# Performance work log

Hardware: AMD Instinct MI355X
Metric: run time of the kernel (lower is better)

The kernel has to match this reference:

```python
import jax, jax.numpy as jnp
import numpy as np

D = 768
NH = 8
HD = D // NH
DFF = 2048
EPS = 1e-5


def _layer_norm(x, g, b):
    mu = jnp.mean(x, axis=-1, keepdims=True)
    var = jnp.mean(jnp.square(x - mu), axis=-1, keepdims=True)
    return (x - mu) * jax.lax.rsqrt(var + EPS) * g + b


def setup_inputs() -> dict:
    key = jax.random.key(0)
    ks = jax.random.split(key, 16)
    B, L = 2, 2048
    s = 0.02
    return {
        "x": jax.random.normal(ks[0], (B, L, D), jnp.float32),
        "attn_bias": jax.random.normal(ks[1], (B, L, L), jnp.float32),
        "in_proj_w": jax.random.normal(ks[2], (3 * D, D), jnp.float32) * s,
        "in_proj_b": jnp.zeros((3 * D,), jnp.float32),
        "out_w": jax.random.normal(ks[3], (D, D), jnp.float32) * s,
        "out_b": jnp.zeros((D,), jnp.float32),
        "W1": jax.random.normal(ks[4], (DFF, D), jnp.float32) * s,
        "b1": jnp.zeros((DFF,), jnp.float32),
        "W2": jax.random.normal(ks[5], (D, DFF), jnp.float32) * s,
        "b2": jnp.zeros((D,), jnp.float32),
        "g1": jnp.ones((D,), jnp.float32),
        "be1": jnp.zeros((D,), jnp.float32),
        "g2": jnp.ones((D,), jnp.float32),
        "be2": jnp.zeros((D,), jnp.float32),
    }


def reference(x, attn_bias, in_proj_w, in_proj_b, out_w, out_b,
              W1, b1, W2, b2, g1, be1, g2, be2):
    B, L, _ = x.shape
    # fused qkv projection (torch nn.MultiheadAttention in_proj)
    qkv = x @ in_proj_w.T + in_proj_b          # [B, L, 3D]
    q, k, v = jnp.split(qkv, 3, axis=-1)
    q = q.reshape(B, L, NH, HD).transpose(0, 2, 1, 3)  # [B, nH, L, hd]
    k = k.reshape(B, L, NH, HD).transpose(0, 2, 1, 3)
    v = v.reshape(B, L, NH, HD).transpose(0, 2, 1, 3)
    scale = 1.0 / jnp.sqrt(jnp.asarray(HD, x.dtype))
    scores = jnp.einsum("bhqd,bhkd->bhqk", q * scale, k)
    scores = scores + attn_bias[:, None, :, :]         # broadcast over heads == expand
    attn = jax.nn.softmax(scores, axis=-1)
    ctx = jnp.einsum("bhqk,bhkd->bhqd", attn, v)       # [B, nH, L, hd]
    ctx = ctx.transpose(0, 2, 1, 3).reshape(B, L, D)
    attn_out = ctx @ out_w.T + out_b
    x = _layer_norm(x + attn_out, g1, be1)
    h = jax.nn.gelu(x @ W1.T + b1, approximate=False)  # torch default GELU = erf
    ff = h @ W2.T + b2
    return _layer_norm(x + ff, g2, be2)
```

## Files before the change

kernel.cpp:

```cpp
#include <hip/hip_runtime.h>
#include <hip/hip_bf16.h>
#include <math.h>

typedef __bf16 bf16;
typedef __attribute__((ext_vector_type(8))) __bf16 bf16x8;
typedef __attribute__((ext_vector_type(4))) __bf16 bf16x4;
typedef __attribute__((ext_vector_type(2))) __bf16 bf16x2;
typedef __attribute__((ext_vector_type(4))) float f32x4;

#define LOG2E 1.4426950408889634f

__device__ __forceinline__ void gload16(const bf16* g, bf16* l) {
  __builtin_amdgcn_global_load_lds(
      (const __attribute__((address_space(1))) void*)g,
      (__attribute__((address_space(3))) void*)l, 16, 0, 0);
}

__device__ __forceinline__ unsigned packbf2(float a, float b) {
  bf16x2 v = { (bf16)a, (bf16)b };
  return __builtin_bit_cast(unsigned, v);
}

struct CastSegs { const float* src[5]; bf16* dst[5]; };

__global__ void fused_cast_kernel(CastSegs segs) {
  const int e0 = 786432, e1 = 1228800, e2 = 1376256, e3 = 1769472, e4 = 2162688;
  int i = blockIdx.x * blockDim.x + threadIdx.x;
  int stride = gridDim.x * blockDim.x;
  for (; i < e4; i += stride) {
    int s = 0, base = 0;
    if (i >= e0) { s = 1; base = e0; }
    if (i >= e1) { s = 2; base = e1; }
    if (i >= e2) { s = 3; base = e2; }
    if (i >= e3) { s = 4; base = e3; }
    float4 v = ((const float4*)segs.src[s])[i - base];
    bf16x4 o = { (bf16)v.x, (bf16)v.y, (bf16)v.z, (bf16)v.w };
    ((bf16x4*)segs.dst[s])[i - base] = o;
  }
}

template<int MODE>
__launch_bounds__(256)
__global__ void gemm_kernel(const bf16* __restrict__ A, const bf16* __restrict__ W,
                            const float* __restrict__ bias, bf16* __restrict__ vt,
                            void* __restrict__ out, int K, int O) {
  __shared__ bf16 As[128 * 64];
  __shared__ bf16 Bs[128 * 64];
  const int t    = threadIdx.x;
  const int lane = t & 63;
  const int wave = t >> 6;
  const int wr = (wave >> 1) * 64;
  const int wc = (wave & 1) * 64;
  const int n0 = blockIdx.y * 128;
  const int o0 = blockIdx.x * 128;

  f32x4 zero = {0.f, 0.f, 0.f, 0.f};
  f32x4 acc[4][4];
#pragma unroll
  for (int m = 0; m < 4; m++)
#pragma unroll
    for (int n = 0; n < 4; n++) acc[m][n] = zero;

  const int fr  = lane & 15;
  const int fg8 = (lane >> 4) * 8;

  for (int k0 = 0; k0 < K; k0 += 64) {
    __syncthreads();
#pragma unroll
    for (int c = 0; c < 4; c++) {
      int f = c * 256 + t;
      int row = f >> 3;
      int col = (f & 7) * 8;
      gload16(&A[(size_t)(n0 + row) * K + k0 + col], &As[f * 8]);
      gload16(&W[(size_t)(o0 + row) * K + k0 + col], &Bs[f * 8]);
    }
    __syncthreads();
#pragma unroll
    for (int kf = 0; kf < 2; kf++) {
      bf16x8 a[4], b[4];
#pragma unroll
      for (int m = 0; m < 4; m++) a[m] = *(const bf16x8*)&As[(wr + m * 16 + fr) * 64 + kf * 32 + fg8];
#pragma unroll
      for (int n = 0; n < 4; n++) b[n] = *(const bf16x8*)&Bs[(wc + n * 16 + fr) * 64 + kf * 32 + fg8];
#pragma unroll
      for (int m = 0; m < 4; m++)
#pragma unroll
        for (int n = 0; n < 4; n++)
          acc[m][n] = __builtin_amdgcn_mfma_f32_16x16x32_bf16(a[m], b[n], acc[m][n], 0, 0, 0);
    }
  }

  const int fg4 = (lane >> 4) * 4;
#pragma unroll
  for (int m = 0; m < 4; m++) {
#pragma unroll
    for (int n = 0; n < 4; n++) {
      int col = o0 + wc + n * 16 + fr;
      float bv = bias[col];
      if constexpr (MODE == 3) {
        if (col >= 1536) {
          int c = col - 1536;
          int h = c / 96;
          int hd = c - h * 96;
          int row0 = n0 + wr + m * 16 + fg4;
          int b = row0 >> 11;
          int token = row0 & 2047;
          bf16x4 ov;
#pragma unroll
          for (int r = 0; r < 4; r++) ov[r] = (bf16)(acc[m][n][r] + bv);
          *(bf16x4*)&vt[((size_t)((b * 8 + h) * 96 + hd)) * 2048 + token] = ov;
          continue;
        }
      }
#pragma unroll
      for (int r = 0; r < 4; r++) {
        int row = n0 + wr + m * 16 + fg4 + r;
        float v = acc[m][n][r] + bv;
        if constexpr (MODE == 2) {
          v = 0.5f * v * (1.0f + erff(v * 0.70710678118654752f));
          ((bf16*)out)[(size_t)row * O + col] = (bf16)v;
        } else {
          ((bf16*)out)[(size_t)row * O + col] = (bf16)v;
        }
      }
    }
  }
}

__launch_bounds__(256)
__global__ void gemmW_kernel(const bf16* __restrict__ A, const bf16* __restrict__ W,
                             const float* __restrict__ bias, const float* __restrict__ res,
                             float* __restrict__ out, int K, int O) {
  __shared__ bf16 As[128 * 64];
  __shared__ bf16 Bs[64 * 64];
  const int t    = threadIdx.x;
  const int lane = t & 63;
  const int wave = t >> 6;
  const int wr = wave * 32;
  const int n0 = blockIdx.y * 128;
  const int o0 = blockIdx.x * 64;

  f32x4 zero = {0.f, 0.f, 0.f, 0.f};
  f32x4 acc[2][4];
#pragma unroll
  for (int m = 0; m < 2; m++)
#pragma unroll
    for (int n = 0; n < 4; n++) acc[m][n] = zero;

  const int fr  = lane & 15;
  const int fg8 = (lane >> 4) * 8;

  for (int k0 = 0; k0 < K; k0 += 64) {
    __syncthreads();
#pragma unroll
    for (int c = 0; c < 4; c++) {
      int f = c * 256 + t;
      int row = f >> 3;
      int col = (f & 7) * 8;
      gload16(&A[(size_t)(n0 + row) * K + k0 + col], &As[f * 8]);
    }
#pragma unroll
    for (int c = 0; c < 2; c++) {
      int f = c * 256 + t;
      int row = f >> 3;
      int col = (f & 7) * 8;
      gload16(&W[(size_t)(o0 + row) * K + k0 + col], &Bs[f * 8]);
    }
    __syncthreads();
#pragma unroll
    for (int kf = 0; kf < 2; kf++) {
      bf16x8 a[2], b[4];
#pragma unroll
      for (int m = 0; m < 2; m++) a[m] = *(const bf16x8*)&As[(wr + m * 16 + fr) * 64 + kf * 32 + fg8];
#pragma unroll
      for (int n = 0; n < 4; n++) b[n] = *(const bf16x8*)&Bs[(n * 16 + fr) * 64 + kf * 32 + fg8];
#pragma unroll
      for (int m = 0; m < 2; m++)
#pragma unroll
        for (int n = 0; n < 4; n++)
          acc[m][n] = __builtin_amdgcn_mfma_f32_16x16x32_bf16(a[m], b[n], acc[m][n], 0, 0, 0);
    }
  }

  const int fg4 = (lane >> 4) * 4;
#pragma unroll
  for (int m = 0; m < 2; m++) {
#pragma unroll
    for (int n = 0; n < 4; n++) {
      int col = o0 + n * 16 + fr;
      float bv = bias[col];
#pragma unroll
      for (int r = 0; r < 4; r++) {
        int row = n0 + wr + m * 16 + fg4 + r;
        float v = acc[m][n][r] + bv + res[(size_t)row * O + col];
        out[(size_t)row * O + col] = v;
      }
    }
  }
}

__launch_bounds__(256, 2)
__global__ void attn_kernel(const bf16* __restrict__ qkv, const bf16* __restrict__ vt,
                            const float* __restrict__ bias, float* __restrict__ opart,
                            float* __restrict__ ml) {
  __shared__ bf16 Ks[64 * 104];
  __shared__ bf16 Vs[96 * 72];
  const int t    = threadIdx.x;
  const int lane = t & 63;
  const int wave = t >> 6;
  const int qb = blockIdx.x, h = blockIdx.y;
  const int half = blockIdx.z & 1, b = blockIdx.z >> 1;
  const int kvstart = half * 1024;
  const int q0 = qb * 128 + wave * 32;
  const int fq = lane & 15;
  const int g  = lane >> 4;
  const size_t base = (size_t)b * 2048 * 2304;

  bf16x8 qf[2][3];
#pragma unroll
  for (int ss = 0; ss < 2; ss++) {
    const bf16* qp = qkv + base + (size_t)(q0 + ss * 16 + fq) * 2304 + h * 96;
#pragma unroll
    for (int f = 0; f < 3; f++) qf[ss][f] = *(const bf16x8*)(qp + f * 32 + g * 8);
  }

  const int krow = t >> 2, kcb = (t & 3) * 24;
  const bf16* kbase = qkv + base + (size_t)kvstart * 2304 + 768 + h * 96;
  const bf16* vbase = vt + (size_t)((b * 8 + h) * 96) * 2048 + kvstart;

  bf16x8 kreg[3], vreg[3];
#pragma unroll
  for (int i = 0; i < 3; i++) {
    kreg[i] = *(const bf16x8*)(kbase + (size_t)krow * 2304 + kcb + i * 8);
    int c = t + 256 * i;
    vreg[i] = *(const bf16x8*)(vbase + (size_t)(c >> 3) * 2048 + (c & 7) * 8);
  }

  float m_run[2] = {-1e30f, -1e30f}, l_run[2] = {0.f, 0.f};
  f32x4 zero = {0.f, 0.f, 0.f, 0.f};
  f32x4 o_acc[2][6];
#pragma unroll
  for (int ss = 0; ss < 2; ss++)
#pragma unroll
    for (int i = 0; i < 6; i++) o_acc[ss][i] = zero;

  const float scale = 0.10206207261596575f;
  const float* bp[2];
  bp[0] = bias + ((size_t)b * 2048 + q0 + fq) * 2048 + kvstart;
  bp[1] = bp[0] + (size_t)16 * 2048;

  bf16x8 pb[2][2];

  for (int kv0 = 0; kv0 < 1024; kv0 += 64) {
    if (kv0) __syncthreads();
    *(bf16x8*)&Ks[krow * 104 + kcb]      = kreg[0];
    *(bf16x8*)&Ks[krow * 104 + kcb + 8]  = kreg[1];
    *(bf16x8*)&Ks[krow * 104 + kcb + 16] = kreg[2];
#pragma unroll
    for (int i = 0; i < 3; i++) {
      int c = t + 256 * i;
      *(bf16x8*)&Vs[(c >> 3) * 72 + (c & 7) * 8] = vreg[i];
    }
    if (kv0 + 64 < 1024) {
      int nx = kv0 + 64;
#pragma unroll
      for (int i = 0; i < 3; i++) {
        kreg[i] = *(const bf16x8*)(kbase + (size_t)(nx + krow) * 2304 + kcb + i * 8);
        int c = t + 256 * i;
        vreg[i] = *(const bf16x8*)(vbase + (size_t)(c >> 3) * 2048 + nx + (c & 7) * 8);
      }
    }
    __builtin_amdgcn_sched_barrier(0);
    __syncthreads();

    float4 bf[2][4];
#pragma unroll
    for (int ss = 0; ss < 2; ss++)
#pragma unroll
      for (int kvt = 0; kvt < 4; kvt++)
        bf[ss][kvt] = *(const float4*)(bp[ss] + kv0 + kvt * 16 + g * 4);

    f32x4 s[2][4];
#pragma unroll
    for (int kvt = 0; kvt < 4; kvt++) {
      s[0][kvt] = zero;
      s[1][kvt] = zero;
#pragma unroll
      for (int f = 0; f < 3; f++) {
        bf16x8 kfr = *(const bf16x8*)&Ks[(kvt * 16 + fq) * 104 + f * 32 + g * 8];
        s[0][kvt] = __builtin_amdgcn_mfma_f32_16x16x32_bf16(kfr, qf[0][f], s[0][kvt], 0, 0, 0);
        s[1][kvt] = __builtin_amdgcn_mfma_f32_16x16x32_bf16(kfr, qf[1][f], s[1][kvt], 0, 0, 0);
      }
    }

#pragma unroll
    for (int ss = 0; ss < 2; ss++) {
      float p[4][4];
      float vmax = -1e30f;
#pragma unroll
      for (int kvt = 0; kvt < 4; kvt++)
#pragma unroll
        for (int r = 0; r < 4; r++) {
          float sv = fmaf(s[ss][kvt][r], scale, (&bf[ss][kvt].x)[r]);
          p[kvt][r] = sv;
          vmax = fmaxf(vmax, sv);
        }
      vmax = fmaxf(vmax, __shfl_xor(vmax, 16));
      vmax = fmaxf(vmax, __shfl_xor(vmax, 32));
      if (!__all(vmax <= m_run[ss] + 8.0f)) {
        float m_new = fmaxf(m_run[ss], vmax);
        float corr = exp2f((m_run[ss] - m_new) * LOG2E);
        l_run[ss] *= corr;
#pragma unroll
        for (int i = 0; i < 6; i++)
#pragma unroll
          for (int r = 0; r < 4; r++) o_acc[ss][i][r] *= corr;
        m_run[ss] = m_new;
      }
      float rsum = 0.f;
      uint2 d[4];
#pragma unroll
      for (int kvt = 0; kvt < 4; kvt++) {
        float e0 = exp2f((p[kvt][0] - m_run[ss]) * LOG2E);
        float e1 = exp2f((p[kvt][1] - m_run[ss]) * LOG2E);
        float e2 = exp2f((p[kvt][2] - m_run[ss]) * LOG2E);
        float e3 = exp2f((p[kvt][3] - m_run[ss]) * LOG2E);
        rsum += (e0 + e1) + (e2 + e3);
        d[kvt].x = packbf2(e0, e1);
        d[kvt].y = packbf2(e2, e3);
      }
      rsum += __shfl_xor(rsum, 16);
      rsum += __shfl_xor(rsum, 32);
      l_run[ss] += rsum;

      bool glow = (g < 2);
      uint2 snd0 = glow ? d[1] : d[0];
      uint2 snd1 = glow ? d[3] : d[2];
      uint2 r0, r1;
      r0.x = __shfl_xor(snd0.x, 32); r0.y = __shfl_xor(snd0.y, 32);
      r1.x = __shfl_xor(snd1.x, 32); r1.y = __shfl_xor(snd1.y, 32);
      uint2 k0 = glow ? d[0] : d[1];
      uint2 k1 = glow ? d[2] : d[3];
      bool sendk = ((g ^ (g >> 1)) & 1);
      uint2 s0 = sendk ? k0 : r0;
      uint2 s1 = sendk ? k1 : r1;
      uint2 q0_, q1_;
      q0_.x = __shfl_xor(s0.x, 16); q0_.y = __shfl_xor(s0.y, 16);
      q1_.x = __shfl_xor(s1.x, 16); q1_.y = __shfl_xor(s1.y, 16);
      uint2 kept0 = sendk ? r0 : k0;
      uint2 kept1 = sendk ? r1 : k1;
      bool godd = (g & 1);
      uint2 lo0 = godd ? q0_ : kept0;
      uint2 hi0 = godd ? kept0 : q0_;
      uint2 lo1 = godd ? q1_ : kept1;
      uint2 hi1 = godd ? kept1 : q1_;
      uint4 u0 = { lo0.x, lo0.y, hi0.x, hi0.y };
      uint4 u1 = { lo1.x, lo1.y, hi1.x, hi1.y };
      pb[ss][0] = __builtin_bit_cast(bf16x8, u0);
      pb[ss][1] = __builtin_bit_cast(bf16x8, u1);
    }

#pragma unroll
    for (int kf = 0; kf < 2; kf++) {
#pragma unroll
      for (int ht = 0; ht < 6; ht++) {
        bf16x8 vfr = *(const bf16x8*)&Vs[(ht * 16 + fq) * 72 + kf * 32 + g * 8];
        o_acc[0][ht] = __builtin_amdgcn_mfma_f32_16x16x32_bf16(vfr, pb[0][kf], o_acc[0][ht], 0, 0, 0);
        o_acc[1][ht] = __builtin_amdgcn_mfma_f32_16x16x32_bf16(vfr, pb[1][kf], o_acc[1][ht], 0, 0, 0);
      }
    }
  }

#pragma unroll
  for (int ss = 0; ss < 2; ss++) {
    int q = q0 + ss * 16 + fq;
    float* op = opart + (size_t)half * (16 * 2048 * 96) + ((size_t)(b * 8 + h) * 2048 + q) * 96;
    float* mlp = ml + ((size_t)half * 32768 + (size_t)(b * 8 + h) * 2048 + q) * 2;
#pragma unroll
    for (int ht = 0; ht < 6; ht++)
      *(f32x4*)&op[ht * 16 + g * 4] = o_acc[ss][ht];
    if (g == 0) { mlp[0] = m_run[ss]; mlp[1] = l_run[ss]; }
  }
}

__launch_bounds__(256)
__global__ void attn_combine_kernel(const float* __restrict__ opart, const float* __restrict__ ml,
                                    bf16* __restrict__ ctx) {
  int idx = blockIdx.x * blockDim.x + threadIdx.x;
  if (idx >= 786432) return;
  int e = idx * 4;
  int bh = e / (2048 * 96);
  int rem = e - bh * (2048 * 96);
  int q = rem / 96;
  int hd = rem - q * 96;
  const float* op0 = opart;
  const float* op1 = opart + (size_t)16 * 2048 * 96;
  float4 o1 = *(const float4*)&op0[e];
  float4 o2 = *(const float4*)&op1[e];
  const float* ml0 = ml + (size_t)(bh * 2048 + q) * 2;
  const float* ml1 = ml0 + (size_t)32768 * 2;
  float m1 = ml0[0], l1 = ml0[1];
  float m2 = ml1[0], l2 = ml1[1];
  float M = fmaxf(m1, m2);
  float w1 = exp2f((m1 - M) * LOG2E);
  float w2 = exp2f((m2 - M) * LOG2E);
  float inv = 1.0f / (l1 * w1 + l2 * w2);
  int b = bh >> 3, h = bh & 7;
  bf16x4 o;
  o[0] = (bf16)((o1.x * w1 + o2.x * w2) * inv);
  o[1] = (bf16)((o1.y * w1 + o2.y * w2) * inv);
  o[2] = (bf16)((o1.z * w1 + o2.z * w2) * inv);
  o[3] = (bf16)((o1.w * w1 + o2.w * w2) * inv);
  *(bf16x4*)&ctx[((size_t)b * 2048 + q) * 768 + h * 96 + hd] = o;
}

__launch_bounds__(256)
__global__ void ln_kernel(const float* in, const float* __restrict__ gamma,
                          const float* __restrict__ beta, float* outf, bf16* outb) {
  const int row = blockIdx.x;
  const int t = threadIdx.x;
  const float* rp = in + (size_t)row * 768;
  float v[3];
#pragma unroll
  for (int i = 0; i < 3; i++) v[i] = rp[t + 256 * i];
  float s = v[0] + v[1] + v[2];
  float ss = v[0] * v[0] + v[1] * v[1] + v[2] * v[2];
#pragma unroll
  for (int off = 1; off < 64; off <<= 1) {
    s += __shfl_xor(s, off);
    ss += __shfl_xor(ss, off);
  }
  __shared__ float red[8];
  if ((t & 63) == 0) { red[(t >> 6) * 2] = s; red[(t >> 6) * 2 + 1] = ss; }
  __syncthreads();
  s = red[0] + red[2] + red[4] + red[6];
  ss = red[1] + red[3] + red[5] + red[7];
  float mu = s * (1.0f / 768.0f);
  float var = ss * (1.0f / 768.0f) - mu * mu;
  float rs = rsqrtf(var + 1e-5f);
#pragma unroll
  for (int i = 0; i < 3; i++) {
    int col = t + 256 * i;
    float y = (v[i] - mu) * rs * gamma[col] + beta[col];
    outf[(size_t)row * 768 + col] = y;
    if (outb) outb[(size_t)row * 768 + col] = (bf16)y;
  }
}

extern "C" void kernel_launch(void* const* d_in, const int* in_sizes, int n_in,
                              void* d_out, int out_size, void* d_ws, size_t ws_size,
                              hipStream_t stream) {
  (void)in_sizes; (void)n_in; (void)out_size; (void)ws_size;
  const float* x     = (const float*)d_in[0];
  const float* ab    = (const float*)d_in[1];
  const float* w_qkv = (const float*)d_in[2];
  const float* b_qkv = (const float*)d_in[3];
  const float* w_out = (const float*)d_in[4];
  const float* b_out = (const float*)d_in[5];
  const float* W1    = (const float*)d_in[6];
  const float* b1    = (const float*)d_in[7];
  const float* W2    = (const float*)d_in[8];
  const float* b2    = (const float*)d_in[9];
  const float* g1    = (const float*)d_in[10];
  const float* be1   = (const float*)d_in[11];
  const float* g2    = (const float*)d_in[12];
  const float* be2   = (const float*)d_in[13];
  float* outf = (float*)d_out;

  char* p = (char*)d_ws;
  bf16* xb    = (bf16*)p;  p += (size_t)4096 * 768 * 2;
  bf16* qkv   = (bf16*)p;  p += (size_t)4096 * 2304 * 2;
  bf16* ctx   = (bf16*)p;  p += (size_t)4096 * 768 * 2;
  float* x1f  = (float*)p; p += (size_t)4096 * 768 * 4;
  bf16* x1b   = (bf16*)p;  p += (size_t)4096 * 768 * 2;
  bf16* hbuf  = (bf16*)p;  p += (size_t)4096 * 2048 * 2;
  bf16* wqkvb = (bf16*)p;  p += (size_t)2304 * 768 * 2;
  bf16* woutb = (bf16*)p;  p += (size_t)768 * 768 * 2;
  bf16* w1b   = (bf16*)p;  p += (size_t)2048 * 768 * 2;
  bf16* w2b   = (bf16*)p;  p += (size_t)768 * 2048 * 2;
  float* opart = (float*)p; p += (size_t)2 * 16 * 2048 * 96 * 4;
  float* mlb   = (float*)p; p += (size_t)2 * 32768 * 2 * 4;
  bf16* vtb   = (bf16*)x1f;

  CastSegs segs;
  segs.src[0] = x;     segs.dst[0] = xb;
  segs.src[1] = w_qkv; segs.dst[1] = wqkvb;
  segs.src[2] = w_out; segs.dst[2] = woutb;
  segs.src[3] = W1;    segs.dst[3] = w1b;
  segs.src[4] = W2;    segs.dst[4] = w2b;
  fused_cast_kernel<<<2048, 256, 0, stream>>>(segs);

  gemm_kernel<3><<<dim3(18, 32), 256, 0, stream>>>(xb, wqkvb, b_qkv, vtb, qkv, 768, 2304);
  attn_kernel<<<dim3(16, 8, 4), 256, 0, stream>>>(qkv, vtb, ab, opart, mlb);
  attn_combine_kernel<<<3072, 256, 0, stream>>>(opart, mlb, ctx);
  gemmW_kernel<<<dim3(12, 32), 256, 0, stream>>>(ctx, woutb, b_out, x, outf, 768, 768);
  ln_kernel<<<4096, 256, 0, stream>>>(outf, g1, be1, x1f, x1b);
  gemm_kernel<2><<<dim3(16, 32), 256, 0, stream>>>(x1b, w1b, b1, nullptr, hbuf, 768, 2048);
  gemmW_kernel<<<dim3(12, 32), 256, 0, stream>>>(hbuf, w2b, b2, x1f, outf, 2048, 768);
  ln_kernel<<<4096, 256, 0, stream>>>(outf, g2, be2, outf, nullptr);
}
```

Measured before the change: 219.9 us.

## Double-buffer K/V tiles and software-pipeline QK^T with previous PV in attention

The attention kernel gets double-buffered shared memory for K and V tiles and a software-pipelined loop. Each iteration issues the QK^T MFMAs for the current tile together with the PV MFMAs for the previous tile's probabilities, so softmax latency can overlap matrix work. LDS use doubles, which may limit occupancy under launch_bounds(256,2). Register pressure also rises from keeping s and pb live across stages.

Result: no change. 222.2 us (+1.1%).

```diff
diff --git a/kernel.cpp b/kernel.cpp
--- a/kernel.cpp
+++ b/kernel.cpp
@@ -203,8 +203,8 @@
 __global__ void attn_kernel(const bf16* __restrict__ qkv, const bf16* __restrict__ vt,
                             const float* __restrict__ bias, float* __restrict__ opart,
                             float* __restrict__ ml) {
-  __shared__ bf16 Ks[64 * 104];
-  __shared__ bf16 Vs[96 * 72];
+  __shared__ bf16 Ks[2][64 * 104];
+  __shared__ bf16 Vs[2][96 * 72];
   const int t    = threadIdx.x;
   const int lane = t & 63;
   const int wave = t >> 6;
@@ -229,12 +229,24 @@
   const bf16* vbase = vt + (size_t)((b * 8 + h) * 96) * 2048 + kvstart;
 
   bf16x8 kreg[3], vreg[3];
-#pragma unroll
-  for (int i = 0; i < 3; i++) {
-    kreg[i] = *(const bf16x8*)(kbase + (size_t)krow * 2304 + kcb + i * 8);
-    int c = t + 256 * i;
-    vreg[i] = *(const bf16x8*)(vbase + (size_t)(c >> 3) * 2048 + (c & 7) * 8);
-  }
+
+#define LOAD_TILE(kv) do { \
+    kreg[0] = *(const bf16x8*)(kbase + (size_t)((kv) + krow) * 2304 + kcb); \
+    kreg[1] = *(const bf16x8*)(kbase + (size_t)((kv) + krow) * 2304 + kcb + 8); \
+    kreg[2] = *(const bf16x8*)(kbase + (size_t)((kv) + krow) * 2304 + kcb + 16); \
+    vreg[0] = *(const bf16x8*)(vbase + (size_t)(t >> 3) * 2048 + (kv) + (t & 7) * 8); \
+    vreg[1] = *(const bf16x8*)(vbase + (size_t)((t >> 3) + 32) * 2048 + (kv) + (t & 7) * 8); \
+    vreg[2] = *(const bf16x8*)(vbase + (size_t)((t >> 3) + 64) * 2048 + (kv) + (t & 7) * 8); \
+  } while (0)
+
+#define STORE_TILE(buf) do { \
+    *(bf16x8*)&Ks[buf][krow * 104 + kcb]      = kreg[0]; \
+    *(bf16x8*)&Ks[buf][krow * 104 + kcb + 8]  = kreg[1]; \
+    *(bf16x8*)&Ks[buf][krow * 104 + kcb + 16] = kreg[2]; \
+    *(bf16x8*)&Vs[buf][((t >> 3)) * 72 + (t & 7) * 8]      = vreg[0]; \
+    *(bf16x8*)&Vs[buf][((t >> 3) + 32) * 72 + (t & 7) * 8] = vreg[1]; \
+    *(bf16x8*)&Vs[buf][((t >> 3) + 64) * 72 + (t & 7) * 8] = vreg[2]; \
+  } while (0)
 
   float m_run[2] = {-1e30f, -1e30f}, l_run[2] = {0.f, 0.f};
   f32x4 zero = {0.f, 0.f, 0.f, 0.f};
@@ -249,127 +261,148 @@
   bp[0] = bias + ((size_t)b * 2048 + q0 + fq) * 2048 + kvstart;
   bp[1] = bp[0] + (size_t)16 * 2048;
 
+  f32x4 s[2][4];
   bf16x8 pb[2][2];
 
-  for (int kv0 = 0; kv0 < 1024; kv0 += 64) {
-    if (kv0) __syncthreads();
-    *(bf16x8*)&Ks[krow * 104 + kcb]      = kreg[0];
-    *(bf16x8*)&Ks[krow * 104 + kcb + 8]  = kreg[1];
-    *(bf16x8*)&Ks[krow * 104 + kcb + 16] = kreg[2];
-#pragma unroll
-    for (int i = 0; i < 3; i++) {
-      int c = t + 256 * i;
-      *(bf16x8*)&Vs[(c >> 3) * 72 + (c & 7) * 8] = vreg[i];
-    }
-    if (kv0 + 64 < 1024) {
-      int nx = kv0 + 64;
-#pragma unroll
-      for (int i = 0; i < 3; i++) {
-        kreg[i] = *(const bf16x8*)(kbase + (size_t)(nx + krow) * 2304 + kcb + i * 8);
-        int c = t + 256 * i;
-        vreg[i] = *(const bf16x8*)(vbase + (size_t)(c >> 3) * 2048 + nx + (c & 7) * 8);
-      }
-    }
-    __builtin_amdgcn_sched_barrier(0);
-    __syncthreads();
-
-    float4 bf[2][4];
+#define QKT(bufidx) do { \
+    _Pragma("unroll") \
+    for (int kvt = 0; kvt < 4; kvt++) { \
+      s[0][kvt] = zero; s[1][kvt] = zero; \
+      _Pragma("unroll") \
+      for (int f = 0; f < 3; f++) { \
+        bf16x8 kfr = *(const bf16x8*)&Ks[bufidx][(kvt * 16 + fq) * 104 + f * 32 + g * 8]; \
+        s[0][kvt] = __builtin_amdgcn_mfma_f32_16x16x32_bf16(kfr, qf[0][f], s[0][kvt], 0, 0, 0); \
+        s[1][kvt] = __builtin_amdgcn_mfma_f32_16x16x32_bf16(kfr, qf[1][f], s[1][kvt], 0, 0, 0); \
+      } \
+    } \
+  } while (0)
+
+#define PV(bufidx) do { \
+    _Pragma("unroll") \
+    for (int kf = 0; kf < 2; kf++) { \
+      _Pragma("unroll") \
+      for (int ht = 0; ht < 6; ht++) { \
+        bf16x8 vfr = *(const bf16x8*)&Vs[bufidx][(ht * 16 + fq) * 72 + kf * 32 + g * 8]; \
+        o_acc[0][ht] = __builtin_amdgcn_mfma_f32_16x16x32_bf16(vfr, pb[0][kf], o_acc[0][ht], 0, 0, 0); \
+        o_acc[1][ht] = __builtin_amdgcn_mfma_f32_16x16x32_bf16(vfr, pb[1][kf], o_acc[1][ht], 0, 0, 0); \
+      } \
+    } \
+  } while (0)
+
+#define SOFTMAX() do { \
+    _Pragma("unroll") \
+    for (int ss = 0; ss < 2; ss++) { \
+      float p[4][4]; \
+      float vmax = -1e30f; \
+      _Pragma("unroll") \
+      for (int kvt = 0; kvt < 4; kvt++) \
+        _Pragma("unroll") \
+        for (int r = 0; r < 4; r++) { \
+          float sv = fmaf(s[ss][kvt][r], scale, (&bfv[ss][kvt].x)[r]); \
+          p[kvt][r] = sv; \
+          vmax = fmaxf(vmax, sv); \
+        } \
+      vmax = fmaxf(vmax, __shfl_xor(vmax, 16)); \
+      vmax = fmaxf(vmax, __shfl_xor(vmax, 32)); \
+      if (!__all(vmax <= m_run[ss] + 8.0f)) { \
+        float m_new = fmaxf(m_run[ss], vmax); \
+        float corr = exp2f((m_run[ss] - m_new) * LOG2E); \
+        l_run[ss] *= corr; \
+        _Pragma("unroll") \
+        for (int i = 0; i < 6; i++) \
+          _Pragma("unroll") \
+          for (int r = 0; r < 4; r++) o_acc[ss][i][r] *= corr; \
+        m_run[ss] = m_new; \
+      } \
+      float rsum = 0.f; \
+      uint2 d[4]; \
+      _Pragma("unroll") \
+      for (int kvt = 0; kvt < 4; kvt++) { \
+        float e0 = exp2f((p[kvt][0] - m_run[ss]) * LOG2E); \
+        float e1 = exp2f((p[kvt][1] - m_run[ss]) * LOG2E); \
+        float e2 = exp2f((p[kvt][2] - m_run[ss]) * LOG2E); \
+        float e3 = exp2f((p[kvt][3] - m_run[ss]) * LOG2E); \
+        rsum += (e0 + e1) + (e2 + e3); \
+        d[kvt].x = packbf2(e0, e1); \
+        d[kvt].y = packbf2(e2, e3); \
+      } \
+      rsum += __shfl_xor(rsum, 16); \
+      rsum += __shfl_xor(rsum, 32); \
+      l_run[ss] += rsum; \
+      bool glow = (g < 2); \
+      uint2 snd0 = glow ? d[1] : d[0]; \
+      uint2 snd1 = glow ? d[3] : d[2]; \
+      uint2 r0, r1; \
+      r0.x = __shfl_xor(snd0.x, 32); r0.y = __shfl_xor(snd0.y, 32); \
+      r1.x = __shfl_xor(snd1.x, 32); r1.y = __shfl_xor(snd1.y, 32); \
+      uint2 k0 = glow ? d[0] : d[1]; \
+      uint2 k1 = glow ? d[2] : d[3]; \
+      bool sendk = ((g ^ (g >> 1)) & 1); \
+      uint2 s0 = sendk ? k0 : r0; \
+      uint2 s1 = sendk ? k1 : r1; \
+      uint2 q0_, q1_; \
+      q0_.x = __shfl_xor(s0.x, 16); q0_.y = __shfl_xor(s0.y, 16); \
+      q1_.x = __shfl_xor(s1.x, 16); q1_.y = __shfl_xor(s1.y, 16); \
+      uint2 kept0 = sendk ? r0 : k0; \
+      uint2 kept1 = sendk ? r1 : k1; \
+      bool godd = (g & 1); \
+      uint2 lo0 = godd ? q0_ : kept0; \
+      uint2 hi0 = godd ? kept0 : q0_; \
+      uint2 lo1 = godd ? q1_ : kept1; \
+      uint2 hi1 = godd ? kept1 : q1_; \
+      uint4 u0 = { lo0.x, lo0.y, hi0.x, hi0.y }; \
+      uint4 u1 = { lo1.x, lo1.y, hi1.x, hi1.y }; \
+      pb[ss][0] = __builtin_bit_cast(bf16x8, u0); \
+      pb[ss][1] = __builtin_bit_cast(bf16x8, u1); \
+    } \
+  } while (0)
+
+  float4 bfv[2][4];
+
+  LOAD_TILE(0);
+  STORE_TILE(0);
+  LOAD_TILE(64);
+  __syncthreads();
+
+#pragma unroll
+  for (int ss = 0; ss < 2; ss++)
+#pragma unroll
+    for (int kvt = 0; kvt < 4; kvt++)
+      bfv[ss][kvt] = *(const float4*)(bp[ss] + kvt * 16 + g * 4);
+  QKT(0);
+  SOFTMAX();
+  STORE_TILE(1);
+  LOAD_TILE(128);
+  __builtin_amdgcn_sched_barrier(0);
+  __syncthreads();
+
+  int cur = 1;
+  for (int i = 1; i < 16; i++) {
+    int kv0 = i * 64;
 #pragma unroll
     for (int ss = 0; ss < 2; ss++)
 #pragma unroll
       for (int kvt = 0; kvt < 4; kvt++)
-        bf[ss][kvt] = *(const float4*)(bp[ss] + kv0 + kvt * 16 + g * 4);
-
-    f32x4 s[2][4];
-#pragma unroll
-    for (int kvt = 0; kvt < 4; kvt++) {
-      s[0][kvt] = zero;
-      s[1][kvt] = zero;
-#pragma unroll
-      for (int f = 0; f < 3; f++) {
-        bf16x8 kfr = *(const bf16x8*)&Ks[(kvt * 16 + fq) * 104 + f * 32 + g * 8];
-        s[0][kvt] = __builtin_amdgcn_mfma_f32_16x16x32_bf16(kfr, qf[0][f], s[0][kvt], 0, 0, 0);
-        s[1][kvt] = __builtin_amdgcn_mfma_f32_16x16x32_bf16(kfr, qf[1][f], s[1][kvt], 0, 0, 0);
-      }
-    }
-
-#pragma unroll
-    for (int ss = 0; ss < 2; ss++) {
-      float p[4][4];
-      float vmax = -1e30f;
-#pragma unroll
-      for (int kvt = 0; kvt < 4; kvt++)
-#pragma unroll
-        for (int r = 0; r < 4; r++) {
-          float sv = fmaf(s[ss][kvt][r], scale, (&bf[ss][kvt].x)[r]);
-          p[kvt][r] = sv;
-          vmax = fmaxf(vmax, sv);
-        }
-      vmax = fmaxf(vmax, __shfl_xor(vmax, 16));
-      vmax = fmaxf(vmax, __shfl_xor(vmax, 32));
-      if (!__all(vmax <= m_run[ss] + 8.0f)) {
-        float m_new = fmaxf(m_run[ss], vmax);
-        float corr = exp2f((m_run[ss] - m_new) * LOG2E);
-        l_run[ss] *= corr;
-#pragma unroll
-        for (int i = 0; i < 6; i++)
-#pragma unroll
-          for (int r = 0; r < 4; r++) o_acc[ss][i][r] *= corr;
-        m_run[ss] = m_new;
-      }
-      float rsum = 0.f;
-      uint2 d[4];
-#pragma unroll
-      for (int kvt = 0; kvt < 4; kvt++) {
-        float e0 = exp2f((p[kvt][0] - m_run[ss]) * LOG2E);
-        float e1 = exp2f((p[kvt][1] - m_run[ss]) * LOG2E);
-        float e2 = exp2f((p[kvt][2] - m_run[ss]) * LOG2E);
-        float e3 = exp2f((p[kvt][3] - m_run[ss]) * LOG2E);
-        rsum += (e0 + e1) + (e2 + e3);
-        d[kvt].x = packbf2(e0, e1);
-        d[kvt].y = packbf2(e2, e3);
-      }
-      rsum += __shfl_xor(rsum, 16);
-      rsum += __shfl_xor(rsum, 32);
-      l_run[ss] += rsum;
-
-      bool glow = (g < 2);
-      uint2 snd0 = glow ? d[1] : d[0];
-      uint2 snd1 = glow ? d[3] : d[2];
-      uint2 r0, r1;
-      r0.x = __shfl_xor(snd0.x, 32); r0.y = __shfl_xor(snd0.y, 32);
-      r1.x = __shfl_xor(snd1.x, 32); r1.y = __shfl_xor(snd1.y, 32);
-      uint2 k0 = glow ? d[0] : d[1];
-      uint2 k1 = glow ? d[2] : d[3];
-      bool sendk = ((g ^ (g >> 1)) & 1);
-      uint2 s0 = sendk ? k0 : r0;
-      uint2 s1 = sendk ? k1 : r1;
-      uint2 q0_, q1_;
-      q0_.x = __shfl_xor(s0.x, 16); q0_.y = __shfl_xor(s0.y, 16);
-      q1_.x = __shfl_xor(s1.x, 16); q1_.y = __shfl_xor(s1.y, 16);
-      uint2 kept0 = sendk ? r0 : k0;
-      uint2 kept1 = sendk ? r1 : k1;
-      bool godd = (g & 1);
-      uint2 lo0 = godd ? q0_ : kept0;
-      uint2 hi0 = godd ? kept0 : q0_;
-      uint2 lo1 = godd ? q1_ : kept1;
-      uint2 hi1 = godd ? kept1 : q1_;
-      uint4 u0 = { lo0.x, lo0.y, hi0.x, hi0.y };
-      uint4 u1 = { lo1.x, lo1.y, hi1.x, hi1.y };
-      pb[ss][0] = __builtin_bit_cast(bf16x8, u0);
-      pb[ss][1] = __builtin_bit_cast(bf16x8, u1);
-    }
-
-#pragma unroll
-    for (int kf = 0; kf < 2; kf++) {
-#pragma unroll
-      for (int ht = 0; ht < 6; ht++) {
-        bf16x8 vfr = *(const bf16x8*)&Vs[(ht * 16 + fq) * 72 + kf * 32 + g * 8];
-        o_acc[0][ht] = __builtin_amdgcn_mfma_f32_16x16x32_bf16(vfr, pb[0][kf], o_acc[0][ht], 0, 0, 0);
-        o_acc[1][ht] = __builtin_amdgcn_mfma_f32_16x16x32_bf16(vfr, pb[1][kf], o_acc[1][ht], 0, 0, 0);
-      }
-    }
-  }
+        bfv[ss][kvt] = *(const float4*)(bp[ss] + kv0 + kvt * 16 + g * 4);
+    QKT(cur);
+    PV(cur ^ 1);
+    SOFTMAX();
+    if (i < 15) {
+      __syncthreads();
+      STORE_TILE(cur ^ 1);
+      if (i < 14) LOAD_TILE((i + 2) * 64);
+      __builtin_amdgcn_sched_barrier(0);
+      __syncthreads();
+    }
+    cur ^= 1;
+  }
+  PV(cur ^ 1);
+
+#undef LOAD_TILE
+#undef STORE_TILE
+#undef QKT
+#undef PV
+#undef SOFTMAX
 
 #pragma unroll
   for (int ss = 0; ss < 2; ss++) {
```

## Halve queries per wave in attention kernel to raise occupancy

Applied to the files above, without the earlier changes.

Each wave in the attention kernel now handles 16 query rows instead of 32, so a block covers 64 queries and the grid doubles. This cuts accumulator and Q-fragment registers, and the launch bound now allows 4 blocks per SM instead of 2 to hide latency. The V tile's LDS padding changes from 72 to 104, which alters its bank-conflict pattern. In exchange, each block reuses the K/V tile loaded into LDS over half as many queries, so K/V global traffic and per-tile softmax overhead per query double.

New measurement: 224.1 us. About the same (+1.9%).

```diff
diff --git a/kernel.cpp b/kernel.cpp
--- a/kernel.cpp
+++ b/kernel.cpp
@@ -199,29 +199,28 @@
   }
 }
 
-__launch_bounds__(256, 2)
+__launch_bounds__(256, 4)
 __global__ void attn_kernel(const bf16* __restrict__ qkv, const bf16* __restrict__ vt,
                             const float* __restrict__ bias, float* __restrict__ opart,
                             float* __restrict__ ml) {
   __shared__ bf16 Ks[64 * 104];
-  __shared__ bf16 Vs[96 * 72];
+  __shared__ bf16 Vs[96 * 104];
   const int t    = threadIdx.x;
   const int lane = t & 63;
   const int wave = t >> 6;
   const int qb = blockIdx.x, h = blockIdx.y;
   const int half = blockIdx.z & 1, b = blockIdx.z >> 1;
   const int kvstart = half * 1024;
-  const int q0 = qb * 128 + wave * 32;
+  const int q0 = qb * 64 + wave * 16;
   const int fq = lane & 15;
   const int g  = lane >> 4;
   const size_t base = (size_t)b * 2048 * 2304;
 
-  bf16x8 qf[2][3];
-#pragma unroll
-  for (int ss = 0; ss < 2; ss++) {
-    const bf16* qp = qkv + base + (size_t)(q0 + ss * 16 + fq) * 2304 + h * 96;
-#pragma unroll
-    for (int f = 0; f < 3; f++) qf[ss][f] = *(const bf16x8*)(qp + f * 32 + g * 8);
+  bf16x8 qf[3];
+  {
+    const bf16* qp = qkv + base + (size_t)(q0 + fq) * 2304 + h * 96;
+#pragma unroll
+    for (int f = 0; f < 3; f++) qf[f] = *(const bf16x8*)(qp + f * 32 + g * 8);
   }
 
   const int krow = t >> 2, kcb = (t & 3) * 24;
@@ -236,20 +235,14 @@
     vreg[i] = *(const bf16x8*)(vbase + (size_t)(c >> 3) * 2048 + (c & 7) * 8);
   }
 
-  float m_run[2] = {-1e30f, -1e30f}, l_run[2] = {0.f, 0.f};
+  float m_run = -1e30f, l_run = 0.f;
   f32x4 zero = {0.f, 0.f, 0.f, 0.f};
-  f32x4 o_acc[2][6];
-#pragma unroll
-  for (int ss = 0; ss < 2; ss++)
-#pragma unroll
-    for (int i = 0; i < 6; i++) o_acc[ss][i] = zero;
+  f32x4 o_acc[6];
+#pragma unroll
+  for (int i = 0; i < 6; i++) o_acc[i] = zero;
 
   const float scale = 0.10206207261596575f;
-  const float* bp[2];
-  bp[0] = bias + ((size_t)b * 2048 + q0 + fq) * 2048 + kvstart;
-  bp[1] = bp[0] + (size_t)16 * 2048;
-
-  bf16x8 pb[2][2];
+  const float* bp = bias + ((size_t)b * 2048 + q0 + fq) * 2048 + kvstart;
 
   for (int kv0 = 0; kv0 < 1024; kv0 += 64) {
     if (kv0) __syncthreads();
@@ -259,7 +252,7 @@
 #pragma unroll
     for (int i = 0; i < 3; i++) {
       int c = t + 256 * i;
-      *(bf16x8*)&Vs[(c >> 3) * 72 + (c & 7) * 8] = vreg[i];
+      *(bf16x8*)&Vs[(c >> 3) * 104 + (c & 7) * 8] = vreg[i];
     }
     if (kv0 + 64 < 1024) {
       int nx = kv0 + 64;
@@ -273,66 +266,62 @@
     __builtin_amdgcn_sched_barrier(0);
     __syncthreads();
 
-    float4 bf[2][4];
-#pragma unroll
-    for (int ss = 0; ss < 2; ss++)
-#pragma unroll
-      for (int kvt = 0; kvt < 4; kvt++)
-        bf[ss][kvt] = *(const float4*)(bp[ss] + kv0 + kvt * 16 + g * 4);
-
-    f32x4 s[2][4];
+    float4 bfv[4];
+#pragma unroll
+    for (int kvt = 0; kvt < 4; kvt++)
+      bfv[kvt] = *(const float4*)(bp + kv0 + kvt * 16 + g * 4);
+
+    f32x4 s[4];
 #pragma unroll
     for (int kvt = 0; kvt < 4; kvt++) {
-      s[0][kvt] = zero;
-      s[1][kvt] = zero;
+      s[kvt] = zero;
 #pragma unroll
       for (int f = 0; f < 3; f++) {
         bf16x8 kfr = *(const bf16x8*)&Ks[(kvt * 16 + fq) * 104 + f * 32 + g * 8];
-        s[0][kvt] = __builtin_amdgcn_mfma_f32_16x16x32_bf16(kfr, qf[0][f], s[0][kvt], 0, 0, 0);
-        s[1][kvt] = __builtin_amdgcn_mfma_f32_16x16x32_bf16(kfr, qf[1][f], s[1][kvt], 0, 0, 0);
-      }
-    }
-
-#pragma unroll
-    for (int ss = 0; ss < 2; ss++) {
-      float p[4][4];
-      float vmax = -1e30f;
-#pragma unroll
-      for (int kvt = 0; kvt < 4; kvt++)
-#pragma unroll
-        for (int r = 0; r < 4; r++) {
-          float sv = fmaf(s[ss][kvt][r], scale, (&bf[ss][kvt].x)[r]);
-          p[kvt][r] = sv;
-          vmax = fmaxf(vmax, sv);
-        }
-      vmax = fmaxf(vmax, __shfl_xor(vmax, 16));
-      vmax = fmaxf(vmax, __shfl_xor(vmax, 32));
-      if (!__all(vmax <= m_run[ss] + 8.0f)) {
-        float m_new = fmaxf(m_run[ss], vmax);
-        float corr = exp2f((m_run[ss] - m_new) * LOG2E);
-        l_run[ss] *= corr;
-#pragma unroll
-        for (int i = 0; i < 6; i++)
-#pragma unroll
-          for (int r = 0; r < 4; r++) o_acc[ss][i][r] *= corr;
-        m_run[ss] = m_new;
-      }
-      float rsum = 0.f;
-      uint2 d[4];
-#pragma unroll
-      for (int kvt = 0; kvt < 4; kvt++) {
-        float e0 = exp2f((p[kvt][0] - m_run[ss]) * LOG2E);
-        float e1 = exp2f((p[kvt][1] - m_run[ss]) * LOG2E);
-        float e2 = exp2f((p[kvt][2] - m_run[ss]) * LOG2E);
-        float e3 = exp2f((p[kvt][3] - m_run[ss]) * LOG2E);
-        rsum += (e0 + e1) + (e2 + e3);
-        d[kvt].x = packbf2(e0, e1);
-        d[kvt].y = packbf2(e2, e3);
-      }
-      rsum += __shfl_xor(rsum, 16);
-      rsum += __shfl_xor(rsum, 32);
-      l_run[ss] += rsum;
-
+        s[kvt] = __builtin_amdgcn_mfma_f32_16x16x32_bf16(kfr, qf[f], s[kvt], 0, 0, 0);
+      }
+    }
+
+    float p[4][4];
+    float vmax = -1e30f;
+#pragma unroll
+    for (int kvt = 0; kvt < 4; kvt++)
+#pragma unroll
+      for (int r = 0; r < 4; r++) {
+        float sv = fmaf(s[kvt][r], scale, (&bfv[kvt].x)[r]);
+        p[kvt][r] = sv;
+        vmax = fmaxf(vmax, sv);
+      }
+    vmax = fmaxf(vmax, __shfl_xor(vmax, 16));
+    vmax = fmaxf(vmax, __shfl_xor(vmax, 32));
+    if (!__all(vmax <= m_run + 8.0f)) {
+      float m_new = fmaxf(m_run, vmax);
+      float corr = exp2f((m_run - m_new) * LOG2E);
+      l_run *= corr;
+#pragma unroll
+      for (int i = 0; i < 6; i++)
+#pragma unroll
+        for (int r = 0; r < 4; r++) o_acc[i][r] *= corr;
+      m_run = m_new;
+    }
+    float rsum = 0.f;
+    uint2 d[4];
+#pragma unroll
+    for (int kvt = 0; kvt < 4; kvt++) {
+      float e0 = exp2f((p[kvt][0] - m_run) * LOG2E);
+      float e1 = exp2f((p[kvt][1] - m_run) * LOG2E);
+      float e2 = exp2f((p[kvt][2] - m_run) * LOG2E);
+      float e3 = exp2f((p[kvt][3] - m_run) * LOG2E);
+      rsum += (e0 + e1) + (e2 + e3);
+      d[kvt].x = packbf2(e0, e1);
+      d[kvt].y = packbf2(e2, e3);
+    }
+    rsum += __shfl_xor(rsum, 16);
+    rsum += __shfl_xor(rsum, 32);
+    l_run += rsum;
+
+    bf16x8 pb[2];
+    {
       bool glow = (g < 2);
       uint2 snd0 = glow ? d[1] : d[0];
       uint2 snd1 = glow ? d[3] : d[2];
@@ -356,30 +345,28 @@
       uint2 hi1 = godd ? kept1 : q1_;
       uint4 u0 = { lo0.x, lo0.y, hi0.x, hi0.y };
       uint4 u1 = { lo1.x, lo1.y, hi1.x, hi1.y };
-      pb[ss][0] = __builtin_bit_cast(bf16x8, u0);
-      pb[ss][1] = __builtin_bit_cast(bf16x8, u1);
+      pb[0] = __builtin_bit_cast(bf16x8, u0);
+      pb[1] = __builtin_bit_cast(bf16x8, u1);
     }
 
 #pragma unroll
     for (int kf = 0; kf < 2; kf++) {
 #pragma unroll
       for (int ht = 0; ht < 6; ht++) {
-        bf16x8 vfr = *(const bf16x8*)&Vs[(ht * 16 + fq) * 72 + kf * 32 + g * 8];
-        o_acc[0][ht] = __builtin_amdgcn_mfma_f32_16x16x32_bf16(vfr, pb[0][kf], o_acc[0][ht], 0, 0, 0);
-        o_acc[1][ht] = __builtin_amdgcn_mfma_f32_16x16x32_bf16(vfr, pb[1][kf], o_acc[1][ht], 0, 0, 0);
-      }
-    }
-  }
-
-#pragma unroll
-  for (int ss = 0; ss < 2; ss++) {
-    int q = q0 + ss * 16 + fq;
+        bf16x8 vfr = *(const bf16x8*)&Vs[(ht * 16 + fq) * 104 + kf * 32 + g * 8];
+        o_acc[ht] = __builtin_amdgcn_mfma_f32_16x16x32_bf16(vfr, pb[kf], o_acc[ht], 0, 0, 0);
+      }
+    }
+  }
+
+  {
+    int q = q0 + fq;
     float* op = opart + (size_t)half * (16 * 2048 * 96) + ((size_t)(b * 8 + h) * 2048 + q) * 96;
     float* mlp = ml + ((size_t)half * 32768 + (size_t)(b * 8 + h) * 2048 + q) * 2;
 #pragma unroll
     for (int ht = 0; ht < 6; ht++)
-      *(f32x4*)&op[ht * 16 + g * 4] = o_acc[ss][ht];
-    if (g == 0) { mlp[0] = m_run[ss]; mlp[1] = l_run[ss]; }
+      *(f32x4*)&op[ht * 16 + g * 4] = o_acc[ht];
+    if (g == 0) { mlp[0] = m_run; mlp[1] = l_run; }
   }
 }
 
@@ -491,7 +478,7 @@
   fused_cast_kernel<<<2048, 256, 0, stream>>>(segs);
 
   gemm_kernel<3><<<dim3(18, 32), 256, 0, stream>>>(xb, wqkvb, b_qkv, vtb, qkv, 768, 2304);
-  attn_kernel<<<dim3(16, 8, 4), 256, 0, stream>>>(qkv, vtb, ab, opart, mlb);
+  attn_kernel<<<dim3(32, 8, 4), 256, 0, stream>>>(qkv, vtb, ab, opart, mlb);
   attn_combine_kernel<<<3072, 256, 0, stream>>>(opart, mlb, ctx);
   gemmW_kernel<<<dim3(12, 32), 256, 0, stream>>>(ctx, woutb, b_out, x, outf, 768, 768);
   ln_kernel<<<4096, 256, 0, stream>>>(outf, g1, be1, x1f, x1b);
```
